# Kernel tuning notes

Hardware: AMD Instinct MI355X
Metric: run time of the kernel (lower is better)

## Reference

```python
import jax, jax.numpy as jnp
import numpy as np

N_NODES = 32768
N_EDGES = 524288
N_FEAT = 256
HID = 256
N_GRAPHS = 64
N_CLASSES = 4
NODES_PER_GRAPH = N_NODES // N_GRAPHS
BN_EPS = 1e-5


def setup_inputs() -> dict:
    key = jax.random.key(0)
    ks = jax.random.split(key, 16)
    x = jax.random.normal(ks[0], (N_NODES, N_FEAT), dtype=jnp.float32)
    edge_index = jax.random.randint(ks[1], (2, N_EDGES), 0, N_NODES, dtype=jnp.int32)
    batch = (jnp.arange(N_NODES, dtype=jnp.int32) // NODES_PER_GRAPH)
    def xavier(k, shape):
        fan_in, fan_out = shape[0], shape[1]
        a = float(np.sqrt(6.0 / (fan_in + fan_out)))
        return jax.random.uniform(k, shape, jnp.float32, -a, a)
    return {
        "x": x, "edge_index": edge_index, "batch": batch,
        "W1": xavier(ks[2], (N_FEAT, HID)), "b1": jnp.zeros((HID,), jnp.float32),
        "g1": jnp.ones((HID,), jnp.float32), "be1": jnp.zeros((HID,), jnp.float32),
        "W2": xavier(ks[3], (HID, HID)), "b2": jnp.zeros((HID,), jnp.float32),
        "g2": jnp.ones((HID,), jnp.float32), "be2": jnp.zeros((HID,), jnp.float32),
        "W_ih": xavier(ks[4], (HID, 4 * HID)), "W_hh": xavier(ks[5], (HID, 4 * HID)),
        "b_ih": jnp.zeros((4 * HID,), jnp.float32), "b_hh": jnp.zeros((4 * HID,), jnp.float32),
        "W_fc": xavier(ks[6], (HID, N_CLASSES)), "b_fc": jnp.zeros((N_CLASSES,), jnp.float32),
    }


def gcn_conv(x, W, b, src, dst):
    # PyG GCNConv: add self-loops, symmetric normalization, aggregate, then bias
    h = x @ W                                   # [N, H]
    deg = jnp.zeros((x.shape[0],), h.dtype).at[dst].add(1.0) + 1.0  # in-deg + self-loop
    dinv = jax.lax.rsqrt(deg)
    coef = dinv[src] * dinv[dst]                # [E]
    msg = h[src] * coef[:, None]                # gather + scale, [E, H]
    agg = jnp.zeros_like(h).at[dst].add(msg)    # scatter-add
    agg = agg + h * (1.0 / deg)[:, None]        # self-loop term (norm = 1/deg)
    return agg + b


def batch_norm(x, gamma, beta):
    mean = jnp.mean(x, axis=0)
    var = jnp.mean(jnp.square(x - mean), axis=0)  # biased, as torch BN training
    return (x - mean) * jax.lax.rsqrt(var + BN_EPS) * gamma + beta


def reference(x, edge_index, batch, W1, b1, g1, be1, W2, b2, g2, be2,
              W_ih, W_hh, b_ih, b_hh, W_fc, b_fc):
    src, dst = edge_index[0], edge_index[1]
    h = jax.nn.relu(batch_norm(gcn_conv(x, W1, b1, src, dst), g1, be1))
    h = jax.nn.relu(batch_norm(gcn_conv(h, W2, b2, src, dst), g2, be2))
    # global mean pool over graphs
    sums = jax.ops.segment_sum(h, batch, num_segments=N_GRAPHS)
    cnts = jax.ops.segment_sum(jnp.ones((h.shape[0],), h.dtype), batch, num_segments=N_GRAPHS)
    pooled = sums / cnts[:, None]               # [G, H]
    # LSTM, seq_len = 1, zero initial state -> single cell step
    h0 = jnp.zeros((N_GRAPHS, HID), h.dtype)
    c0 = jnp.zeros((N_GRAPHS, HID), h.dtype)
    gates = pooled @ W_ih + h0 @ W_hh + b_ih + b_hh  # [G, 4H]
    i, f, g, o = jnp.split(gates, 4, axis=1)
    c1 = jax.nn.sigmoid(f) * c0 + jax.nn.sigmoid(i) * jnp.tanh(g)
    h1 = jax.nn.sigmoid(o) * jnp.tanh(c1)
    logits = h1 @ W_fc + b_fc
    logp = jax.nn.log_softmax(logits, axis=1)
    return (logp, (h1[None], c1[None]))
```

## Files before the change

### kernel.cpp

```cpp
#include <hip/hip_runtime.h>
#include <math.h>

#define N_NODES 32768
#define N_FEAT 256
#define HID 256
#define N_GRAPHS 64
#define NPG 512
#define N_CLASSES 4
#define BN_EPS 1e-5f

typedef __attribute__((ext_vector_type(8))) short bf16x8;
typedef __attribute__((ext_vector_type(4))) float f32x4;

__device__ __forceinline__ ushort f2b(float f) {
    union { float f; uint u; } v; v.f = f;
    uint u = v.u;
    return (ushort)((u + 0x7FFFu + ((u >> 16) & 1u)) >> 16);
}
__device__ __forceinline__ float bflo(uint u) {
    union { uint u; float f; } v; v.u = u << 16;
    return v.f;
}
__device__ __forceinline__ float bfhi(uint u) {
    union { uint u; float f; } v; v.u = u & 0xFFFF0000u;
    return v.f;
}

__global__ void k_count(const int* __restrict__ dst, int* __restrict__ degcnt, int E) {
    int e = blockIdx.x * 256 + threadIdx.x;
    if (e < E) atomicAdd(&degcnt[dst[e]], 1);
}

__global__ __launch_bounds__(1024) void k_scan_all(const int* __restrict__ degcnt,
                                                   float* __restrict__ dinv,
                                                   int* __restrict__ row_start,
                                                   int* __restrict__ cursor) {
    __shared__ int wsum[16];
    int t = threadIdx.x;
    int base = t * 32;
    int s = 0;
#pragma unroll
    for (int i = 0; i < 32; ++i) s += degcnt[base + i];
    int lane = t & 63, w = t >> 6;
    int v = s;
    for (int off = 1; off < 64; off <<= 1) {
        int u = __shfl_up(v, off);
        if (lane >= off) v += u;
    }
    if (lane == 63) wsum[w] = v;
    __syncthreads();
    if (t < 16) {
        int x = wsum[t];
        for (int off = 1; off < 16; off <<= 1) {
            int u = __shfl_up(x, off, 16);
            if (t >= off) x += u;
        }
        wsum[t] = x;
    }
    __syncthreads();
    int run = ((w > 0) ? wsum[w - 1] : 0) + v - s;
    for (int i = 0; i < 32; ++i) {
        int n = base + i;
        int c = degcnt[n];
        row_start[n] = run;
        cursor[n] = run;
        dinv[n] = rsqrtf((float)(c + 1));
        run += c;
    }
    if (t == 0) row_start[N_NODES] = wsum[15];
}

__global__ void k_fill(const int* __restrict__ src, const int* __restrict__ dst,
                       int* __restrict__ cursor, uint* __restrict__ csrs, int E) {
    int e = blockIdx.x * 256 + threadIdx.x;
    if (e >= E) return;
    int d = dst[e];
    int pos = atomicAdd(&cursor[d], 1);
    csrs[pos] = (uint)src[e];
}

__global__ void k_prep(const float* __restrict__ x, ushort* __restrict__ xb, int n8blk,
                       const float* __restrict__ W1, const float* __restrict__ W2,
                       ushort* __restrict__ Wt1, ushort* __restrict__ Wt2) {
    int b = blockIdx.x;
    if (b < n8blk) {
        int i = b * 256 + threadIdx.x;
        float4 v0 = *(const float4*)(x + (size_t)i * 8);
        float4 v1 = *(const float4*)(x + (size_t)i * 8 + 4);
        uint4 o;
        o.x = (uint)f2b(v0.x) | ((uint)f2b(v0.y) << 16);
        o.y = (uint)f2b(v0.z) | ((uint)f2b(v0.w) << 16);
        o.z = (uint)f2b(v1.x) | ((uint)f2b(v1.y) << 16);
        o.w = (uint)f2b(v1.z) | ((uint)f2b(v1.w) << 16);
        *(uint4*)(xb + (size_t)i * 8) = o;
    } else {
        int wb = b - n8blk;
        const float* W = (wb < 256) ? W1 : W2;
        ushort* Wt = (wb < 256) ? Wt1 : Wt2;
        int n = wb & 255;
        int k = threadIdx.x;
        Wt[n * 256 + k] = f2b(W[k * 256 + n]);
    }
}

__global__ __launch_bounds__(256) void k_gemm_bf16(const ushort* __restrict__ A,
                                                   const ushort* __restrict__ Bt,
                                                   const float* __restrict__ dinv,
                                                   ushort* __restrict__ hs) {
    int wid = threadIdx.x >> 6;
    int lane = threadIdx.x & 63;
    int m0 = blockIdx.y * 256 + wid * 64;
    int n0 = blockIdx.x * 64;
    int r = lane & 15;
    int ko = (lane >> 4) * 8;

    const ushort* Ab = A + (size_t)(m0 + r) * 256 + ko;
    const ushort* Bb = Bt + (size_t)(n0 + r) * 256 + ko;

    f32x4 acc[4][4] = {};
#pragma unroll
    for (int ks = 0; ks < 8; ++ks) {
        bf16x8 a[4], b[4];
#pragma unroll
        for (int i = 0; i < 4; ++i) {
            a[i] = *(const bf16x8*)(Ab + i * (16 * 256) + ks * 32);
            b[i] = *(const bf16x8*)(Bb + i * (16 * 256) + ks * 32);
        }
#pragma unroll
        for (int i = 0; i < 4; ++i)
#pragma unroll
            for (int j = 0; j < 4; ++j)
                acc[i][j] = __builtin_amdgcn_mfma_f32_16x16x32_bf16(a[i], b[j], acc[i][j], 0, 0, 0);
    }

    int rr = (lane >> 4) * 4;
    int cc = lane & 15;
#pragma unroll
    for (int i = 0; i < 4; ++i) {
        int row = m0 + i * 16 + rr;
#pragma unroll
        for (int r2 = 0; r2 < 4; ++r2) {
            float dv = dinv[row + r2];
#pragma unroll
            for (int j = 0; j < 4; ++j) {
                int col = n0 + j * 16 + cc;
                hs[(size_t)(row + r2) * 256 + col] = f2b(acc[i][j][r2] * dv);
            }
        }
    }
}

__global__ __launch_bounds__(256) void k_agg(const ushort* __restrict__ hs,
                                             const uint* __restrict__ csrs,
                                             const int* __restrict__ row_start,
                                             const float* __restrict__ dinv,
                                             const float* __restrict__ bias,
                                             ushort* __restrict__ aggb) {
    int wid = threadIdx.x >> 6;
    int lane = threadIdx.x & 63;
    int foff = lane * 4;
    int n = blockIdx.x * 4 + wid;

    float dv = dinv[n];
    int base = row_start[n];
    int cnt = row_start[n + 1] - base;

    uint2 hv = *(const uint2*)(hs + (size_t)n * 256 + foff);
    float a0 = bflo(hv.x), a1 = bfhi(hv.x), a2 = bflo(hv.y), a3 = bfhi(hv.y);

    int j = 0;
    for (; j + 8 <= cnt; j += 8) {
        uint s0 = csrs[base + j + 0];
        uint s1 = csrs[base + j + 1];
        uint s2 = csrs[base + j + 2];
        uint s3 = csrs[base + j + 3];
        uint s4 = csrs[base + j + 4];
        uint s5 = csrs[base + j + 5];
        uint s6 = csrs[base + j + 6];
        uint s7 = csrs[base + j + 7];
        uint2 h0 = *(const uint2*)(hs + (size_t)s0 * 256 + foff);
        uint2 h1 = *(const uint2*)(hs + (size_t)s1 * 256 + foff);
        uint2 h2 = *(const uint2*)(hs + (size_t)s2 * 256 + foff);
        uint2 h3 = *(const uint2*)(hs + (size_t)s3 * 256 + foff);
        uint2 h4 = *(const uint2*)(hs + (size_t)s4 * 256 + foff);
        uint2 h5 = *(const uint2*)(hs + (size_t)s5 * 256 + foff);
        uint2 h6 = *(const uint2*)(hs + (size_t)s6 * 256 + foff);
        uint2 h7 = *(const uint2*)(hs + (size_t)s7 * 256 + foff);
        a0 += bflo(h0.x) + bflo(h1.x) + bflo(h2.x) + bflo(h3.x)
            + bflo(h4.x) + bflo(h5.x) + bflo(h6.x) + bflo(h7.x);
        a1 += bfhi(h0.x) + bfhi(h1.x) + bfhi(h2.x) + bfhi(h3.x)
            + bfhi(h4.x) + bfhi(h5.x) + bfhi(h6.x) + bfhi(h7.x);
        a2 += bflo(h0.y) + bflo(h1.y) + bflo(h2.y) + bflo(h3.y)
            + bflo(h4.y) + bflo(h5.y) + bflo(h6.y) + bflo(h7.y);
        a3 += bfhi(h0.y) + bfhi(h1.y) + bfhi(h2.y) + bfhi(h3.y)
            + bfhi(h4.y) + bfhi(h5.y) + bfhi(h6.y) + bfhi(h7.y);
    }
    for (; j + 2 <= cnt; j += 2) {
        uint s0 = csrs[base + j + 0];
        uint s1 = csrs[base + j + 1];
        uint2 h0 = *(const uint2*)(hs + (size_t)s0 * 256 + foff);
        uint2 h1 = *(const uint2*)(hs + (size_t)s1 * 256 + foff);
        a0 += bflo(h0.x) + bflo(h1.x);
        a1 += bfhi(h0.x) + bfhi(h1.x);
        a2 += bflo(h0.y) + bflo(h1.y);
        a3 += bfhi(h0.y) + bfhi(h1.y);
    }
    if (j < cnt) {
        uint s0 = csrs[base + j];
        uint2 h0 = *(const uint2*)(hs + (size_t)s0 * 256 + foff);
        a0 += bflo(h0.x); a1 += bfhi(h0.x);
        a2 += bflo(h0.y); a3 += bfhi(h0.y);
    }

    float4 bv = *(const float4*)&bias[foff];
    ushort4 ov;
    ov.x = f2b(a0 * dv + bv.x);
    ov.y = f2b(a1 * dv + bv.y);
    ov.z = f2b(a2 * dv + bv.z);
    ov.w = f2b(a3 * dv + bv.w);
    *(ushort4*)(aggb + (size_t)n * HID + foff) = ov;
}

__global__ __launch_bounds__(256) void k_bn_stats_b(const ushort* __restrict__ aggb,
                                                    float* __restrict__ bnsum,
                                                    float* __restrict__ bnsq) {
    int f = threadIdx.x;
    int r0 = blockIdx.x * 32;
    float s = 0.0f, q = 0.0f;
#pragma unroll 4
    for (int r = 0; r < 32; ++r) {
        float v = bflo((uint)aggb[(size_t)(r0 + r) * HID + f]);
        s += v;
        q += v * v;
    }
    atomicAdd(&bnsum[f], s);
    atomicAdd(&bnsq[f], q);
}

__global__ void k_bn_apply_b(const ushort* __restrict__ x, const float* __restrict__ bnsum,
                             const float* __restrict__ bnsq, const float* __restrict__ gamma,
                             const float* __restrict__ beta, ushort* __restrict__ out) {
    int i = blockIdx.x * 256 + threadIdx.x;
    if (i >= N_NODES * HID / 4) return;
    int f = (i & 63) * 4;
    const float invN = 1.0f / (float)N_NODES;
    uint2 v = *(const uint2*)(x + (size_t)i * 4);
    float vv[4] = {bflo(v.x), bfhi(v.x), bflo(v.y), bfhi(v.y)};
    float r[4];
#pragma unroll
    for (int qq = 0; qq < 4; ++qq) {
        float mean = bnsum[f + qq] * invN;
        float var = bnsq[f + qq] * invN - mean * mean;
        float t = (vv[qq] - mean) * rsqrtf(var + BN_EPS) * gamma[f + qq] + beta[f + qq];
        r[qq] = t > 0.0f ? t : 0.0f;
    }
    uint2 o;
    o.x = (uint)f2b(r[0]) | ((uint)f2b(r[1]) << 16);
    o.y = (uint)f2b(r[2]) | ((uint)f2b(r[3]) << 16);
    *(uint2*)(out + (size_t)i * 4) = o;
}

__global__ __launch_bounds__(256) void k_bn_pool(const ushort* __restrict__ aggb,
                                                 const float* __restrict__ bnsum,
                                                 const float* __restrict__ bnsq,
                                                 const float* __restrict__ gamma,
                                                 const float* __restrict__ beta,
                                                 float* __restrict__ pooled) {
    int g = blockIdx.x >> 4;
    int blk = blockIdx.x & 15;
    int f = threadIdx.x;
    const float invN = 1.0f / (float)N_NODES;
    float mean = bnsum[f] * invN;
    float var = bnsq[f] * invN - mean * mean;
    float sc = rsqrtf(var + BN_EPS) * gamma[f];
    float sh = beta[f] - mean * sc;
    int r0 = g * NPG + blk * 32;
    float s = 0.0f;
#pragma unroll 4
    for (int r = 0; r < 32; ++r) {
        float v = bflo((uint)aggb[(size_t)(r0 + r) * HID + f]) * sc + sh;
        s += v > 0.0f ? v : 0.0f;
    }
    atomicAdd(&pooled[g * HID + f], s);
}

__global__ __launch_bounds__(256) void k_head(const float* __restrict__ pooled,
                                              const float* __restrict__ W_ih,
                                              const float* __restrict__ b_ih,
                                              const float* __restrict__ b_hh,
                                              const float* __restrict__ W_fc,
                                              const float* __restrict__ b_fc,
                                              float* __restrict__ out) {
    __shared__ float p[HID];
    __shared__ float lsum[N_CLASSES][256];
    __shared__ float logits[N_CLASSES];
    int g = blockIdx.x, j = threadIdx.x;
    p[j] = pooled[g * HID + j] * (1.0f / (float)NPG);
    __syncthreads();

    float gi = 0.f, gf = 0.f, gg = 0.f, go = 0.f;
#pragma unroll 4
    for (int k = 0; k < HID; ++k) {
        float pk = p[k];
        const float* w = &W_ih[(size_t)k * (4 * HID) + j];
        gi += pk * w[0];
        gf += pk * w[HID];
        gg += pk * w[2 * HID];
        go += pk * w[3 * HID];
    }
    gi += b_ih[j] + b_hh[j];
    gf += b_ih[HID + j] + b_hh[HID + j];
    gg += b_ih[2 * HID + j] + b_hh[2 * HID + j];
    go += b_ih[3 * HID + j] + b_hh[3 * HID + j];
    (void)gf;

    float si = 1.f / (1.f + expf(-gi));
    float so = 1.f / (1.f + expf(-go));
    float c1 = si * tanhf(gg);
    float h1 = so * tanhf(c1);

    out[N_GRAPHS * N_CLASSES + g * HID + j] = h1;
    out[N_GRAPHS * N_CLASSES + N_GRAPHS * HID + g * HID + j] = c1;

#pragma unroll
    for (int c = 0; c < N_CLASSES; ++c)
        lsum[c][j] = h1 * W_fc[j * N_CLASSES + c];
    __syncthreads();
    for (int s = 128; s > 0; s >>= 1) {
        if (j < s) {
#pragma unroll
            for (int c = 0; c < N_CLASSES; ++c)
                lsum[c][j] += lsum[c][j + s];
        }
        __syncthreads();
    }
    if (j < N_CLASSES) logits[j] = lsum[j][0] + b_fc[j];
    __syncthreads();
    if (j < N_CLASSES) {
        float m = fmaxf(fmaxf(logits[0], logits[1]), fmaxf(logits[2], logits[3]));
        float lse = m + logf(expf(logits[0] - m) + expf(logits[1] - m) +
                             expf(logits[2] - m) + expf(logits[3] - m));
        out[g * N_CLASSES + j] = logits[j] - lse;
    }
}

extern "C" void kernel_launch(void* const* d_in, const int* in_sizes, int n_in,
                              void* d_out, int out_size, void* d_ws, size_t ws_size,
                              hipStream_t stream) {
    const float* x    = (const float*)d_in[0];
    const int*   ei   = (const int*)d_in[1];
    const float* W1   = (const float*)d_in[3];
    const float* b1   = (const float*)d_in[4];
    const float* g1   = (const float*)d_in[5];
    const float* be1  = (const float*)d_in[6];
    const float* W2   = (const float*)d_in[7];
    const float* b2   = (const float*)d_in[8];
    const float* g2   = (const float*)d_in[9];
    const float* be2  = (const float*)d_in[10];
    const float* W_ih = (const float*)d_in[11];
    const float* b_ih = (const float*)d_in[13];
    const float* b_hh = (const float*)d_in[14];
    const float* W_fc = (const float*)d_in[15];
    const float* b_fc = (const float*)d_in[16];
    float* out = (float*)d_out;

    int E = in_sizes[1] / 2;
    const int* src = ei;
    const int* dst = ei + E;

    const size_t MAT = (size_t)N_NODES * HID;
    ushort* aggb = (ushort*)d_ws;
    ushort* xb   = aggb + MAT;
    ushort* hs   = xb + MAT;
    ushort* Wt1  = hs + MAT;
    ushort* Wt2  = Wt1 + 65536;
    float*  dinv = (float*)(Wt2 + 65536);
    int*    row_start = (int*)(dinv + N_NODES);
    int*    cursor    = row_start + N_NODES + 1;
    uint*   csrs      = (uint*)(cursor + N_NODES);
    int*    degcnt = (int*)(csrs + E);
    float*  bn1sum = (float*)(degcnt + N_NODES);
    float*  bn1sq  = bn1sum + HID;
    float*  bn2sum = bn1sq + HID;
    float*  bn2sq  = bn2sum + HID;
    float*  pooled = bn2sq + HID;
    size_t zeroBytes = (size_t)N_NODES * 4 + 4 * HID * 4 + (size_t)N_GRAPHS * HID * 4;

    dim3 blk(256);
    int edgeBlocks = (E + 255) / 256;
    int n8blk = (int)(MAT / 8 / 256);
    int vec4Blocks = (int)(MAT / 4 / 256);
    int aggBlocks = N_NODES / 4;
    dim3 gemmGrid(HID / 64, N_NODES / 256);

    hipMemsetAsync(degcnt, 0, zeroBytes, stream);

    k_count<<<edgeBlocks, blk, 0, stream>>>(dst, degcnt, E);
    k_scan_all<<<1, dim3(1024), 0, stream>>>(degcnt, dinv, row_start, cursor);
    k_fill<<<edgeBlocks, blk, 0, stream>>>(src, dst, cursor, csrs, E);
    k_prep<<<n8blk + 512, blk, 0, stream>>>(x, xb, n8blk, W1, W2, Wt1, Wt2);

    k_gemm_bf16<<<gemmGrid, blk, 0, stream>>>(xb, Wt1, dinv, hs);
    k_agg<<<aggBlocks, blk, 0, stream>>>(hs, csrs, row_start, dinv, b1, aggb);
    k_bn_stats_b<<<N_NODES / 32, blk, 0, stream>>>(aggb, bn1sum, bn1sq);
    k_bn_apply_b<<<vec4Blocks, blk, 0, stream>>>(aggb, bn1sum, bn1sq, g1, be1, xb);

    k_gemm_bf16<<<gemmGrid, blk, 0, stream>>>(xb, Wt2, dinv, hs);
    k_agg<<<aggBlocks, blk, 0, stream>>>(hs, csrs, row_start, dinv, b2, aggb);
    k_bn_stats_b<<<N_NODES / 32, blk, 0, stream>>>(aggb, bn2sum, bn2sq);
    k_bn_pool<<<N_GRAPHS * 16, blk, 0, stream>>>(aggb, bn2sum, bn2sq, g2, be2, pooled);

    k_head<<<N_GRAPHS, blk, 0, stream>>>(pooled, W_ih, b_ih, b_hh, W_fc, b_fc, out);
}
```

Baseline: 319.3 us.

## Fuse CSR build with prep/GEMM, pad rows to pairs, widen aggregation and BN stats

Merges the degree count, bf16 conversion and sentinel init into one launch, and runs the CSR fill alongside the first GEMM in a single grid. Each CSR row gets the self-loop as its first entry and is padded to an even length with a sentinel that points at a zero row. This lets the aggregation have two half-waves each load 16-byte vectors, then reduce across the halves with a shuffle. The GEMM gets an XCD-aware block mapping, and BN stats use vectorized loads with a shared-memory reduction so fewer atomics are issued. In exchange there is extra padded gather traffic, the CSR buffer is larger, and the fused kernels have more complex block scheduling.

```diff
diff --git a/kernel.cpp b/kernel.cpp
--- a/kernel.cpp
+++ b/kernel.cpp
@@ -26,65 +26,18 @@
     return v.f;
 }
 
-__global__ void k_count(const int* __restrict__ dst, int* __restrict__ degcnt, int E) {
-    int e = blockIdx.x * 256 + threadIdx.x;
-    if (e < E) atomicAdd(&degcnt[dst[e]], 1);
-}
-
-__global__ __launch_bounds__(1024) void k_scan_all(const int* __restrict__ degcnt,
-                                                   float* __restrict__ dinv,
-                                                   int* __restrict__ row_start,
-                                                   int* __restrict__ cursor) {
-    __shared__ int wsum[16];
+__global__ void k_count_prep(const int* __restrict__ dst, int* __restrict__ degcnt, int cntB,
+                             const float* __restrict__ x, ushort* __restrict__ xb, int xB,
+                             const float* __restrict__ W1, const float* __restrict__ W2,
+                             ushort* __restrict__ Wt1, ushort* __restrict__ Wt2,
+                             uint* __restrict__ csrs, int E) {
+    int b = blockIdx.x;
     int t = threadIdx.x;
-    int base = t * 32;
-    int s = 0;
-#pragma unroll
-    for (int i = 0; i < 32; ++i) s += degcnt[base + i];
-    int lane = t & 63, w = t >> 6;
-    int v = s;
-    for (int off = 1; off < 64; off <<= 1) {
-        int u = __shfl_up(v, off);
-        if (lane >= off) v += u;
-    }
-    if (lane == 63) wsum[w] = v;
-    __syncthreads();
-    if (t < 16) {
-        int x = wsum[t];
-        for (int off = 1; off < 16; off <<= 1) {
-            int u = __shfl_up(x, off, 16);
-            if (t >= off) x += u;
-        }
-        wsum[t] = x;
-    }
-    __syncthreads();
-    int run = ((w > 0) ? wsum[w - 1] : 0) + v - s;
-    for (int i = 0; i < 32; ++i) {
-        int n = base + i;
-        int c = degcnt[n];
-        row_start[n] = run;
-        cursor[n] = run;
-        dinv[n] = rsqrtf((float)(c + 1));
-        run += c;
-    }
-    if (t == 0) row_start[N_NODES] = wsum[15];
-}
-
-__global__ void k_fill(const int* __restrict__ src, const int* __restrict__ dst,
-                       int* __restrict__ cursor, uint* __restrict__ csrs, int E) {
-    int e = blockIdx.x * 256 + threadIdx.x;
-    if (e >= E) return;
-    int d = dst[e];
-    int pos = atomicAdd(&cursor[d], 1);
-    csrs[pos] = (uint)src[e];
-}
-
-__global__ void k_prep(const float* __restrict__ x, ushort* __restrict__ xb, int n8blk,
-                       const float* __restrict__ W1, const float* __restrict__ W2,
-                       ushort* __restrict__ Wt1, ushort* __restrict__ Wt2) {
-    int b = blockIdx.x;
-    if (b < n8blk) {
-        int i = b * 256 + threadIdx.x;
+    if (b < cntB) {
+        int e = b * 256 + t;
+        if (e < E) atomicAdd(&degcnt[dst[e]], 1);
+    } else if (b < cntB + xB) {
+        int i = (b - cntB) * 256 + t;
         float4 v0 = *(const float4*)(x + (size_t)i * 8);
         float4 v1 = *(const float4*)(x + (size_t)i * 8 + 4);
         uint4 o;
@@ -93,24 +46,87 @@
         o.z = (uint)f2b(v1.x) | ((uint)f2b(v1.y) << 16);
         o.w = (uint)f2b(v1.z) | ((uint)f2b(v1.w) << 16);
         *(uint4*)(xb + (size_t)i * 8) = o;
-    } else {
-        int wb = b - n8blk;
+    } else if (b < cntB + xB + 512) {
+        int wb = b - cntB - xB;
         const float* W = (wb < 256) ? W1 : W2;
         ushort* Wt = (wb < 256) ? Wt1 : Wt2;
         int n = wb & 255;
-        int k = threadIdx.x;
-        Wt[n * 256 + k] = f2b(W[k * 256 + n]);
-    }
-}
-
-__global__ __launch_bounds__(256) void k_gemm_bf16(const ushort* __restrict__ A,
-                                                   const ushort* __restrict__ Bt,
-                                                   const float* __restrict__ dinv,
-                                                   ushort* __restrict__ hs) {
+        Wt[n * 256 + t] = f2b(W[t * 256 + n]);
+    } else {
+        int i = (b - cntB - xB - 512) * 256 + t;
+        uint4 s = make_uint4(N_NODES, N_NODES, N_NODES, N_NODES);
+        *(uint4*)(csrs + (size_t)i * 4) = s;
+    }
+}
+
+__global__ __launch_bounds__(1024) void k_scan_all(const int* __restrict__ degcnt,
+                                                   float* __restrict__ dinv,
+                                                   int* __restrict__ row_start,
+                                                   int* __restrict__ cursor,
+                                                   uint* __restrict__ csrs,
+                                                   ushort* __restrict__ hs_pad) {
+    __shared__ int wsum[16];
+    int t = threadIdx.x;
+    int base = t * 32;
+    int s = 0;
+#pragma unroll
+    for (int i = 0; i < 32; ++i) {
+        int c = degcnt[base + i];
+        s += (c + 2) & ~1;
+    }
+    int lane = t & 63, w = t >> 6;
+    int v = s;
+    for (int off = 1; off < 64; off <<= 1) {
+        int u = __shfl_up(v, off);
+        if (lane >= off) v += u;
+    }
+    if (lane == 63) wsum[w] = v;
+    __syncthreads();
+    if (t < 16) {
+        int x = wsum[t];
+        for (int off = 1; off < 16; off <<= 1) {
+            int u = __shfl_up(x, off, 16);
+            if (t >= off) x += u;
+        }
+        wsum[t] = x;
+    }
+    __syncthreads();
+    int run = ((w > 0) ? wsum[w - 1] : 0) + v - s;
+    for (int i = 0; i < 32; ++i) {
+        int n = base + i;
+        int c = degcnt[n];
+        row_start[n] = run;
+        csrs[run] = (uint)n;
+        cursor[n] = run + 1;
+        dinv[n] = rsqrtf((float)(c + 1));
+        run += (c + 2) & ~1;
+    }
+    if (t == 0) row_start[N_NODES] = wsum[15];
+    if (t < 128) ((uint*)hs_pad)[t] = 0;
+}
+
+__device__ __forceinline__ void fill_body(int e, const int* __restrict__ src,
+                                          const int* __restrict__ dst,
+                                          int* __restrict__ cursor, uint* __restrict__ csrs,
+                                          int E) {
+    if (e >= E) return;
+    int d = dst[e];
+    int pos = atomicAdd(&cursor[d], 1);
+    csrs[pos] = (uint)src[e];
+}
+
+__device__ __forceinline__ void gemm_body(int bid, const ushort* __restrict__ A,
+                                          const ushort* __restrict__ Bt,
+                                          const float* __restrict__ dinv,
+                                          ushort* __restrict__ hs) {
     int wid = threadIdx.x >> 6;
     int lane = threadIdx.x & 63;
-    int m0 = blockIdx.y * 256 + wid * 64;
-    int n0 = blockIdx.x * 64;
+    int xcd = bid & 7;
+    int slot = bid >> 3;
+    int cb = slot & 3;
+    int pr = xcd + ((slot >> 2) << 3);
+    int m0 = pr * 256 + wid * 64;
+    int n0 = cb * 64;
     int r = lane & 15;
     int ko = (lane >> 4) * 8;
 
@@ -148,6 +164,29 @@
             }
         }
     }
+}
+
+__global__ __launch_bounds__(256) void k_fill_gemm1(const ushort* __restrict__ A,
+                                                    const ushort* __restrict__ Bt,
+                                                    const float* __restrict__ dinv,
+                                                    ushort* __restrict__ hs,
+                                                    const int* __restrict__ src,
+                                                    const int* __restrict__ dst,
+                                                    int* __restrict__ cursor,
+                                                    uint* __restrict__ csrs, int E) {
+    int b = blockIdx.x;
+    if (b < 512) {
+        gemm_body(b, A, Bt, dinv, hs);
+    } else {
+        fill_body((b - 512) * 256 + threadIdx.x, src, dst, cursor, csrs, E);
+    }
+}
+
+__global__ __launch_bounds__(256) void k_gemm2(const ushort* __restrict__ A,
+                                               const ushort* __restrict__ Bt,
+                                               const float* __restrict__ dinv,
+                                               ushort* __restrict__ hs) {
+    gemm_body(blockIdx.x, A, Bt, dinv, hs);
 }
 
 __global__ __launch_bounds__(256) void k_agg(const ushort* __restrict__ hs,
@@ -158,83 +197,102 @@
                                              ushort* __restrict__ aggb) {
     int wid = threadIdx.x >> 6;
     int lane = threadIdx.x & 63;
-    int foff = lane * 4;
+    int half = lane >> 5;
+    int fq = lane & 31;
     int n = blockIdx.x * 4 + wid;
 
     float dv = dinv[n];
     int base = row_start[n];
-    int cnt = row_start[n + 1] - base;
-
-    uint2 hv = *(const uint2*)(hs + (size_t)n * 256 + foff);
-    float a0 = bflo(hv.x), a1 = bfhi(hv.x), a2 = bflo(hv.y), a3 = bfhi(hv.y);
-
-    int j = 0;
-    for (; j + 8 <= cnt; j += 8) {
-        uint s0 = csrs[base + j + 0];
-        uint s1 = csrs[base + j + 1];
-        uint s2 = csrs[base + j + 2];
-        uint s3 = csrs[base + j + 3];
-        uint s4 = csrs[base + j + 4];
-        uint s5 = csrs[base + j + 5];
-        uint s6 = csrs[base + j + 6];
-        uint s7 = csrs[base + j + 7];
-        uint2 h0 = *(const uint2*)(hs + (size_t)s0 * 256 + foff);
-        uint2 h1 = *(const uint2*)(hs + (size_t)s1 * 256 + foff);
-        uint2 h2 = *(const uint2*)(hs + (size_t)s2 * 256 + foff);
-        uint2 h3 = *(const uint2*)(hs + (size_t)s3 * 256 + foff);
-        uint2 h4 = *(const uint2*)(hs + (size_t)s4 * 256 + foff);
-        uint2 h5 = *(const uint2*)(hs + (size_t)s5 * 256 + foff);
-        uint2 h6 = *(const uint2*)(hs + (size_t)s6 * 256 + foff);
-        uint2 h7 = *(const uint2*)(hs + (size_t)s7 * 256 + foff);
-        a0 += bflo(h0.x) + bflo(h1.x) + bflo(h2.x) + bflo(h3.x)
-            + bflo(h4.x) + bflo(h5.x) + bflo(h6.x) + bflo(h7.x);
-        a1 += bfhi(h0.x) + bfhi(h1.x) + bfhi(h2.x) + bfhi(h3.x)
-            + bfhi(h4.x) + bfhi(h5.x) + bfhi(h6.x) + bfhi(h7.x);
-        a2 += bflo(h0.y) + bflo(h1.y) + bflo(h2.y) + bflo(h3.y)
-            + bflo(h4.y) + bflo(h5.y) + bflo(h6.y) + bflo(h7.y);
-        a3 += bfhi(h0.y) + bfhi(h1.y) + bfhi(h2.y) + bfhi(h3.y)
-            + bfhi(h4.y) + bfhi(h5.y) + bfhi(h6.y) + bfhi(h7.y);
-    }
-    for (; j + 2 <= cnt; j += 2) {
-        uint s0 = csrs[base + j + 0];
-        uint s1 = csrs[base + j + 1];
-        uint2 h0 = *(const uint2*)(hs + (size_t)s0 * 256 + foff);
-        uint2 h1 = *(const uint2*)(hs + (size_t)s1 * 256 + foff);
-        a0 += bflo(h0.x) + bflo(h1.x);
-        a1 += bfhi(h0.x) + bfhi(h1.x);
-        a2 += bflo(h0.y) + bflo(h1.y);
-        a3 += bfhi(h0.y) + bfhi(h1.y);
-    }
-    if (j < cnt) {
-        uint s0 = csrs[base + j];
-        uint2 h0 = *(const uint2*)(hs + (size_t)s0 * 256 + foff);
+    int pairs = (row_start[n + 1] - base) >> 1;
+
+    float a0 = 0.f, a1 = 0.f, a2 = 0.f, a3 = 0.f, a4 = 0.f, a5 = 0.f, a6 = 0.f, a7 = 0.f;
+
+    int t = 0;
+    for (; t + 4 <= pairs; t += 4) {
+        uint s0 = csrs[base + 2 * t + 0 + half];
+        uint s1 = csrs[base + 2 * t + 2 + half];
+        uint s2 = csrs[base + 2 * t + 4 + half];
+        uint s3 = csrs[base + 2 * t + 6 + half];
+        uint4 h0 = *(const uint4*)(hs + (size_t)s0 * 256 + fq * 8);
+        uint4 h1 = *(const uint4*)(hs + (size_t)s1 * 256 + fq * 8);
+        uint4 h2 = *(const uint4*)(hs + (size_t)s2 * 256 + fq * 8);
+        uint4 h3 = *(const uint4*)(hs + (size_t)s3 * 256 + fq * 8);
+        a0 += bflo(h0.x) + bflo(h1.x) + bflo(h2.x) + bflo(h3.x);
+        a1 += bfhi(h0.x) + bfhi(h1.x) + bfhi(h2.x) + bfhi(h3.x);
+        a2 += bflo(h0.y) + bflo(h1.y) + bflo(h2.y) + bflo(h3.y);
+        a3 += bfhi(h0.y) + bfhi(h1.y) + bfhi(h2.y) + bfhi(h3.y);
+        a4 += bflo(h0.z) + bflo(h1.z) + bflo(h2.z) + bflo(h3.z);
+        a5 += bfhi(h0.z) + bfhi(h1.z) + bfhi(h2.z) + bfhi(h3.z);
+        a6 += bflo(h0.w) + bflo(h1.w) + bflo(h2.w) + bflo(h3.w);
+        a7 += bfhi(h0.w) + bfhi(h1.w) + bfhi(h2.w) + bfhi(h3.w);
+    }
+    for (; t < pairs; ++t) {
+        uint s0 = csrs[base + 2 * t + half];
+        uint4 h0 = *(const uint4*)(hs + (size_t)s0 * 256 + fq * 8);
         a0 += bflo(h0.x); a1 += bfhi(h0.x);
         a2 += bflo(h0.y); a3 += bfhi(h0.y);
-    }
-
-    float4 bv = *(const float4*)&bias[foff];
-    ushort4 ov;
-    ov.x = f2b(a0 * dv + bv.x);
-    ov.y = f2b(a1 * dv + bv.y);
-    ov.z = f2b(a2 * dv + bv.z);
-    ov.w = f2b(a3 * dv + bv.w);
-    *(ushort4*)(aggb + (size_t)n * HID + foff) = ov;
-}
-
-__global__ __launch_bounds__(256) void k_bn_stats_b(const ushort* __restrict__ aggb,
-                                                    float* __restrict__ bnsum,
-                                                    float* __restrict__ bnsq) {
-    int f = threadIdx.x;
-    int r0 = blockIdx.x * 32;
-    float s = 0.0f, q = 0.0f;
-#pragma unroll 4
-    for (int r = 0; r < 32; ++r) {
-        float v = bflo((uint)aggb[(size_t)(r0 + r) * HID + f]);
-        s += v;
-        q += v * v;
-    }
-    atomicAdd(&bnsum[f], s);
-    atomicAdd(&bnsq[f], q);
+        a4 += bflo(h0.z); a5 += bfhi(h0.z);
+        a6 += bflo(h0.w); a7 += bfhi(h0.w);
+    }
+
+    a0 += __shfl_xor(a0, 32); a1 += __shfl_xor(a1, 32);
+    a2 += __shfl_xor(a2, 32); a3 += __shfl_xor(a3, 32);
+    a4 += __shfl_xor(a4, 32); a5 += __shfl_xor(a5, 32);
+    a6 += __shfl_xor(a6, 32); a7 += __shfl_xor(a7, 32);
+
+    if (half == 0) {
+        float4 b0 = *(const float4*)&bias[fq * 8];
+        float4 b1 = *(const float4*)&bias[fq * 8 + 4];
+        float o0 = a0 * dv + b0.x, o1 = a1 * dv + b0.y;
+        float o2 = a2 * dv + b0.z, o3 = a3 * dv + b0.w;
+        float o4 = a4 * dv + b1.x, o5 = a5 * dv + b1.y;
+        float o6 = a6 * dv + b1.z, o7 = a7 * dv + b1.w;
+        uint4 ov;
+        ov.x = (uint)f2b(o0) | ((uint)f2b(o1) << 16);
+        ov.y = (uint)f2b(o2) | ((uint)f2b(o3) << 16);
+        ov.z = (uint)f2b(o4) | ((uint)f2b(o5) << 16);
+        ov.w = (uint)f2b(o6) | ((uint)f2b(o7) << 16);
+        *(uint4*)(aggb + (size_t)n * HID + fq * 8) = ov;
+    }
+}
+
+__global__ __launch_bounds__(256) void k_bn_stats(const ushort* __restrict__ aggb,
+                                                  float* __restrict__ bnsum,
+                                                  float* __restrict__ bnsq) {
+    int t = threadIdx.x;
+    int fq = t & 31;
+    int rg = t >> 5;
+    int r0 = blockIdx.x * 128 + rg * 16;
+
+    float s[8] = {}, q[8] = {};
+    for (int r = 0; r < 16; ++r) {
+        uint4 v = *(const uint4*)(aggb + (size_t)(r0 + r) * HID + fq * 8);
+        float f0 = bflo(v.x), f1 = bfhi(v.x), f2 = bflo(v.y), f3 = bfhi(v.y);
+        float f4 = bflo(v.z), f5 = bfhi(v.z), f6 = bflo(v.w), f7 = bfhi(v.w);
+        s[0] += f0; q[0] += f0 * f0;  s[1] += f1; q[1] += f1 * f1;
+        s[2] += f2; q[2] += f2 * f2;  s[3] += f3; q[3] += f3 * f3;
+        s[4] += f4; q[4] += f4 * f4;  s[5] += f5; q[5] += f5 * f5;
+        s[6] += f6; q[6] += f6 * f6;  s[7] += f7; q[7] += f7 * f7;
+    }
+
+    __shared__ float red[8][32][16];
+#pragma unroll
+    for (int i = 0; i < 8; ++i) {
+        red[rg][fq][i] = s[i];
+        red[rg][fq][8 + i] = q[i];
+    }
+    __syncthreads();
+    int fq2 = t & 31;
+    int vg = t >> 5;
+#pragma unroll
+    for (int k = 0; k < 2; ++k) {
+        int v = vg * 2 + k;
+        float acc = 0.f;
+#pragma unroll
+        for (int rgi = 0; rgi < 8; ++rgi) acc += red[rgi][fq2][v];
+        float* dstp = (v < 8) ? bnsum : bnsq;
+        atomicAdd(&dstp[fq2 * 8 + (v & 7)], acc);
+    }
 }
 
 __global__ void k_bn_apply_b(const ushort* __restrict__ x, const float* __restrict__ bnsum,
@@ -369,16 +427,18 @@
     const int* dst = ei + E;
 
     const size_t MAT = (size_t)N_NODES * HID;
+    size_t SZ = ((size_t)E + 2 * N_NODES + 1023) & ~(size_t)1023;
+
     ushort* aggb = (ushort*)d_ws;
     ushort* xb   = aggb + MAT;
     ushort* hs   = xb + MAT;
-    ushort* Wt1  = hs + MAT;
+    ushort* Wt1  = hs + MAT + 256;
     ushort* Wt2  = Wt1 + 65536;
     float*  dinv = (float*)(Wt2 + 65536);
     int*    row_start = (int*)(dinv + N_NODES);
-    int*    cursor    = row_start + N_NODES + 1;
+    int*    cursor    = row_start + N_NODES + 2;
     uint*   csrs      = (uint*)(cursor + N_NODES);
-    int*    degcnt = (int*)(csrs + E);
+    int*    degcnt = (int*)(csrs + SZ);
     float*  bn1sum = (float*)(degcnt + N_NODES);
     float*  bn1sq  = bn1sum + HID;
     float*  bn2sum = bn1sq + HID;
@@ -389,25 +449,26 @@
     dim3 blk(256);
     int edgeBlocks = (E + 255) / 256;
     int n8blk = (int)(MAT / 8 / 256);
+    int sentB = (int)(SZ / 1024);
     int vec4Blocks = (int)(MAT / 4 / 256);
     int aggBlocks = N_NODES / 4;
-    dim3 gemmGrid(HID / 64, N_NODES / 256);
 
     hipMemsetAsync(degcnt, 0, zeroBytes, stream);
 
-    k_count<<<edgeBlocks, blk, 0, stream>>>(dst, degcnt, E);
-    k_scan_all<<<1, dim3(1024), 0, stream>>>(degcnt, dinv, row_start, cursor);
-    k_fill<<<edgeBlocks, blk, 0, stream>>>(src, dst, cursor, csrs, E);
-    k_prep<<<n8blk + 512, blk, 0, stream>>>(x, xb, n8blk, W1, W2, Wt1, Wt2);
-
-    k_gemm_bf16<<<gemmGrid, blk, 0, stream>>>(xb, Wt1, dinv, hs);
+    k_count_prep<<<edgeBlocks + n8blk + 512 + sentB, blk, 0, stream>>>(
+        dst, degcnt, edgeBlocks, x, xb, n8blk, W1, W2, Wt1, Wt2, csrs, E);
+    k_scan_all<<<1, dim3(1024), 0, stream>>>(degcnt, dinv, row_start, cursor, csrs,
+                                             hs + MAT);
+
+    k_fill_gemm1<<<512 + edgeBlocks, blk, 0, stream>>>(xb, Wt1, dinv, hs,
+                                                       src, dst, cursor, csrs, E);
     k_agg<<<aggBlocks, blk, 0, stream>>>(hs, csrs, row_start, dinv, b1, aggb);
-    k_bn_stats_b<<<N_NODES / 32, blk, 0, stream>>>(aggb, bn1sum, bn1sq);
+    k_bn_stats<<<N_NODES / 128, blk, 0, stream>>>(aggb, bn1sum, bn1sq);
     k_bn_apply_b<<<vec4Blocks, blk, 0, stream>>>(aggb, bn1sum, bn1sq, g1, be1, xb);
 
-    k_gemm_bf16<<<gemmGrid, blk, 0, stream>>>(xb, Wt2, dinv, hs);
+    k_gemm2<<<512, blk, 0, stream>>>(xb, Wt2, dinv, hs);
     k_agg<<<aggBlocks, blk, 0, stream>>>(hs, csrs, row_start, dinv, b2, aggb);
-    k_bn_stats_b<<<N_NODES / 32, blk, 0, stream>>>(aggb, bn2sum, bn2sq);
+    k_bn_stats<<<N_NODES / 128, blk, 0, stream>>>(aggb, bn2sum, bn2sq);
     k_bn_pool<<<N_GRAPHS * 16, blk, 0, stream>>>(aggb, bn2sum, bn2sq, g2, be2, pooled);
 
     k_head<<<N_GRAPHS, blk, 0, stream>>>(pooled, W_ih, b_ih, b_hh, W_fc, b_fc, out);
```

Result: slower. 336.2 us (+5.3%).
